# Kernel tuning notes

Hardware: AMD Instinct MI355X
Metric: run time of the kernel (lower is better)

## Reference

```python
import jax, jax.numpy as jnp
import numpy as np

N_HEAD = 12

def setup_inputs() -> dict:
    key = jax.random.key(0)
    k1, k2, k3 = jax.random.split(key, 3)
    B, T, E = 4, 2048, 768
    x = jax.random.normal(k1, (B, T, E), dtype=jnp.float32)
    Wqkv = jax.random.normal(k2, (E, 3 * E), dtype=jnp.float32) * 0.02
    Wproj = jax.random.normal(k3, (E, E), dtype=jnp.float32) * 0.02
    return {"x": x, "Wqkv": Wqkv, "Wproj": Wproj}

def reference(x, Wqkv, Wproj):
    B, T, E = x.shape
    H = N_HEAD
    hd = E // H
    qkv = x @ Wqkv                                  # [B,T,3E]
    q, k, v = jnp.split(qkv, 3, axis=-1)
    # [B,T,E] -> [B,H,T,hd]
    q = q.reshape(B, T, H, hd).transpose(0, 2, 1, 3)
    k = k.reshape(B, T, H, hd).transpose(0, 2, 1, 3)
    v = v.reshape(B, T, H, hd).transpose(0, 2, 1, 3)
    scores = jnp.einsum("bhqd,bhkd->bhqk", q, k) / jnp.sqrt(jnp.float32(hd))
    # original: masked_fill(tril(scores)==0, -inf) == causal mask (upper triangle zeroed by tril)
    masked = jnp.where(jnp.tril(scores) == 0, -jnp.inf, scores)
    attn = jax.nn.softmax(masked, axis=-1)
    out = jnp.einsum("bhqk,bhkd->bhqd", attn, v)    # [B,H,T,hd]
    out = out.transpose(0, 2, 1, 3).reshape(B, T, E)
    return out @ Wproj
```

## Files before the change

### kernel.cpp

```cpp
#include <hip/hip_runtime.h>
#include <hip/hip_bf16.h>


#define BB 4
#define TT 2048
#define EE 768
#define HH 12
#define HD 64
#define KK 768
#define BTE (BB*TT*EE)

typedef __attribute__((ext_vector_type(8))) short bf16x8;
typedef __attribute__((ext_vector_type(4))) float f32x4;
typedef __attribute__((ext_vector_type(16))) float f32x16;
typedef __attribute__((ext_vector_type(4))) int i32x4;

#define QSC 0.18033688011112042f

#define GLOAD16(gp, lp) \
    __builtin_amdgcn_global_load_lds( \
        (const __attribute__((address_space(1))) unsigned*)(gp), \
        (__attribute__((address_space(3))) unsigned*)(lp), 16, 0, 0)

static __device__ __forceinline__ unsigned short f2bf(float f) {
    unsigned u = __builtin_bit_cast(unsigned, f);
    u += 0x7fffu + ((u >> 16) & 1u);
    return (unsigned short)(u >> 16);
}

static __device__ __forceinline__ unsigned cvt_pk_bf16(float lo, float hi) {
    unsigned r;
    asm("v_cvt_pk_bf16_f32 %0, %1, %2" : "=v"(r) : "v"(lo), "v"(hi));
    return r;
}

__global__ __launch_bounds__(256)
void convx_kernel(const float* __restrict__ x, unsigned short* __restrict__ xb) {
    const size_t i = ((size_t)blockIdx.x * 256 + threadIdx.x) * 8;
    float4 a = *(const float4*)&x[i];
    float4 b = *(const float4*)&x[i + 4];
    ushort4 lo, hi;
    lo.x = f2bf(a.x); lo.y = f2bf(a.y); lo.z = f2bf(a.z); lo.w = f2bf(a.w);
    hi.x = f2bf(b.x); hi.y = f2bf(b.y); hi.z = f2bf(b.z); hi.w = f2bf(b.w);
    *(ushort4*)&xb[i] = lo;
    *(ushort4*)&xb[i + 4] = hi;
}

__global__ __launch_bounds__(256)
void transw_kernel(const float* __restrict__ W, unsigned short* __restrict__ Wt, int N) {
    __shared__ unsigned short Ts[64][72];
    const int n0 = blockIdx.x * 64;
    const int k0 = blockIdx.y * 64;
    const int tid = threadIdx.x;
    {
        const int r = tid >> 4;
        const int c4 = (tid & 15) << 2;
#pragma unroll
        for (int i = 0; i < 4; ++i) {
            const int k = r + i * 16;
            float4 w4 = *(const float4*)&W[(size_t)(k0 + k) * N + n0 + c4];
            Ts[k][c4 + 0] = f2bf(w4.x); Ts[k][c4 + 1] = f2bf(w4.y);
            Ts[k][c4 + 2] = f2bf(w4.z); Ts[k][c4 + 3] = f2bf(w4.w);
        }
    }
    __syncthreads();
#pragma unroll
    for (int i = 0; i < 2; ++i) {
        const int idx = tid + i * 256;
        const int n = idx >> 3;
        const int ch = idx & 7;
        ushort4 p0, p1;
        p0.x = Ts[ch * 8 + 0][n]; p0.y = Ts[ch * 8 + 1][n];
        p0.z = Ts[ch * 8 + 2][n]; p0.w = Ts[ch * 8 + 3][n];
        p1.x = Ts[ch * 8 + 4][n]; p1.y = Ts[ch * 8 + 5][n];
        p1.z = Ts[ch * 8 + 6][n]; p1.w = Ts[ch * 8 + 7][n];
        *(ushort4*)&Wt[(size_t)(n0 + n) * KK + k0 + ch * 8] = p0;
        *(ushort4*)&Wt[(size_t)(n0 + n) * KK + k0 + ch * 8 + 4] = p1;
    }
}

template<int MODE>
__global__ __launch_bounds__(256)
void mfma_gemm_kernel(const unsigned short* __restrict__ A,
                      const unsigned short* __restrict__ Wt,
                      unsigned short* __restrict__ q_ws,
                      unsigned short* __restrict__ k_ws,
                      unsigned short* __restrict__ v_ws,
                      float* __restrict__ outf) {
    __shared__ __align__(16) unsigned short As[3][8 * 512];
    __shared__ __align__(16) unsigned short Bs[3][8 * 512];

    const int nwg = gridDim.x * gridDim.y;
    const int orig = blockIdx.y * gridDim.x + blockIdx.x;
    const int cpx = nwg >> 3;
    const int swz = (orig & 7) * cpx + (orig >> 3);
    const int bx = swz % gridDim.x;
    const int by = swz / gridDim.x;

    const int tid = threadIdx.x;
    const int w = tid >> 6, lane = tid & 63;
    const int c = lane & 15, g = lane >> 4;
    const int wr = w >> 1, wc = w & 1;
    const int m0 = by * 128, n0 = bx * 128;

    const int lrow16 = lane & 15;
    const int lch16  = (lane >> 4) * 8;

    const unsigned short* Ap = A  + (size_t)m0 * KK;
    const unsigned short* Bp = Wt + (size_t)n0 * KK;

    f32x4 acc[4][4] = {};
    const int NT = KK / 32;

#define GSTAGE(pp, kt_) do { const int k0_ = (kt_) * 32; const int f0_ = 2 * w; \
        GLOAD16(Ap + (size_t)(f0_ * 16      + lrow16) * KK + k0_ + lch16, &As[pp][(f0_    ) * 512]); \
        GLOAD16(Ap + (size_t)((f0_ + 1) * 16 + lrow16) * KK + k0_ + lch16, &As[pp][(f0_ + 1) * 512]); \
        GLOAD16(Bp + (size_t)(f0_ * 16      + lrow16) * KK + k0_ + lch16, &Bs[pp][(f0_    ) * 512]); \
        GLOAD16(Bp + (size_t)((f0_ + 1) * 16 + lrow16) * KK + k0_ + lch16, &Bs[pp][(f0_ + 1) * 512]); \
    } while (0)

    GSTAGE(0, 0);
    GSTAGE(1, 1);

    for (int kt = 0; kt < NT; ++kt) {
        if (kt < NT - 1) asm volatile("s_waitcnt vmcnt(4)" ::: "memory");
        else             asm volatile("s_waitcnt vmcnt(0)" ::: "memory");
        __builtin_amdgcn_s_barrier();
        __builtin_amdgcn_sched_barrier(0);
        asm volatile("" ::: "memory");

        if (kt + 2 < NT) GSTAGE((kt + 2) % 3, kt + 2);

        const int p = kt % 3;
        bf16x8 af[4], bfr[4];
#pragma unroll
        for (int m = 0; m < 4; ++m)
            af[m] = *(const bf16x8*)&As[p][(wr * 4 + m) * 512 + lane * 8];
#pragma unroll
        for (int n = 0; n < 4; ++n)
            bfr[n] = *(const bf16x8*)&Bs[p][(wc * 4 + n) * 512 + lane * 8];
#pragma unroll
        for (int m = 0; m < 4; ++m)
#pragma unroll
            for (int n = 0; n < 4; ++n)
                acc[m][n] = __builtin_amdgcn_mfma_f32_16x16x32_bf16(af[m], bfr[n], acc[m][n], 0, 0, 0);
    }
#undef GSTAGE

    if (MODE == 0) {
        const int which = n0 / EE;
        const int hh = (n0 % EE) / HD + wc;
        const int bb = m0 / TT;
        const int tb = (m0 % TT) + wr * 64;
        const int bh = bb * HH + hh;
        if (which < 2) {
            const float sc_ = (which == 0) ? QSC : 1.0f;
            unsigned short* dst = (which == 0) ? q_ws : k_ws;
#pragma unroll
            for (int m = 0; m < 4; ++m) {
                const int t32 = (tb >> 5) + (m >> 1);
#pragma unroll
                for (int n = 0; n < 4; ++n) {
                    unsigned short* base = dst
                        + ((size_t)(bh * (TT / 32) + t32) * 4 + n) * 512
                        + ((m & 1) * 16 + 4 * g + 32 * (c >> 3)) * 8 + (c & 7);
#pragma unroll
                    for (int j = 0; j < 4; ++j)
                        base[j * 8] = f2bf(acc[m][n][j] * sc_);
                }
            }
        } else {
            unsigned short* vb = v_ws + ((size_t)(bh * (TT / 64) + (tb >> 6))) * 4096;
#pragma unroll
            for (int m = 0; m < 4; ++m)
#pragma unroll
                for (int n = 0; n < 4; ++n) {
                    unsigned short* base = vb + ((size_t)(n >> 1) * 4 + m) * 512
                        + ((n & 1) * 16 + c + 32 * (g >> 1)) * 8 + 4 * (g & 1);
                    ushort4 pk;
                    pk.x = f2bf(acc[m][n][0]); pk.y = f2bf(acc[m][n][1]);
                    pk.z = f2bf(acc[m][n][2]); pk.w = f2bf(acc[m][n][3]);
                    *(ushort4*)base = pk;
                }
        }
    } else {
#pragma unroll
        for (int m = 0; m < 4; ++m)
#pragma unroll
            for (int n = 0; n < 4; ++n)
#pragma unroll
                for (int j = 0; j < 4; ++j)
                    outf[(size_t)(m0 + wr * 64 + m * 16 + 4 * g + j) * EE
                         + n0 + wc * 64 + n * 16 + c] = acc[m][n][j];
    }
}

__global__ __launch_bounds__(64)
void attn_kernel(const unsigned short* __restrict__ qf,
                 const unsigned short* __restrict__ kfr,
                 const unsigned short* __restrict__ vfr,
                 unsigned short* __restrict__ attn_b) {
    const int bh = blockIdx.x;
    const int j = (TT / 32 - 1) - (int)blockIdx.y;
    const int b = bh / HH, h = bh % HH;
    const int lane = threadIdx.x;
    const int lq = lane & 31;
    const int hiL = lane >> 5;

    const int q0 = j * 32;
    const int qg = q0 + lq;

    const unsigned short* qbase = qf + ((size_t)(bh * (TT / 32) + j)) * 2048;
    bf16x8 qa[4];
#pragma unroll
    for (int ds = 0; ds < 4; ++ds)
        qa[ds] = *(const bf16x8*)&qbase[ds * 512 + lane * 8];

    const unsigned short* kfb = kfr + (size_t)bh * 131072;
    const unsigned short* vfb = vfr + (size_t)bh * 131072;

    const i32x4 onesw = {0x3F803F80, 0x3F803F80, 0x3F803F80, 0x3F803F80};
    const bf16x8 ones = __builtin_bit_cast(bf16x8, onesw);

    f32x16 o0 = {}, o1 = {}, ol = {};

    const int ktiles = (j >> 1) + 1;

    for (int kt = 0; kt < ktiles; ++kt) {
        const int kv0 = kt * 64;

        bf16x8 kf[8], vf[8];
        {
            const unsigned short* kc = kfb + ((size_t)(2 * kt) * 4) * 512 + lane * 8;
#pragma unroll
            for (int ch = 0; ch < 8; ++ch)
                kf[ch] = *(const bf16x8*)&kc[ch * 512];
            const unsigned short* vc = vfb + (size_t)kt * 4096 + lane * 8;
#pragma unroll
            for (int ch = 0; ch < 8; ++ch)
                vf[ch] = *(const bf16x8*)&vc[ch * 512];
        }

        f32x16 s0 = {}, s1 = {};
        __builtin_amdgcn_s_setprio(1);
#pragma unroll
        for (int ds = 0; ds < 4; ++ds) {
            s0 = __builtin_amdgcn_mfma_f32_32x32x16_bf16(kf[ds],     qa[ds], s0, 0, 0, 0);
            s1 = __builtin_amdgcn_mfma_f32_32x32x16_bf16(kf[4 + ds], qa[ds], s1, 0, 0, 0);
        }
        __builtin_amdgcn_s_setprio(0);

        if (kv0 + 63 > q0) {
#pragma unroll
            for (int r = 0; r < 16; ++r) {
                const int crow = (r & 3) + 8 * (r >> 2) + 4 * hiL;
                if (kv0 + crow > qg)      s0[r] = -INFINITY;
                if (kv0 + 32 + crow > qg) s1[r] = -INFINITY;
            }
        }

#pragma unroll
        for (int r = 0; r < 16; ++r) s0[r] = __builtin_amdgcn_exp2f(s0[r]);
#pragma unroll
        for (int r = 0; r < 16; ++r) s1[r] = __builtin_amdgcn_exp2f(s1[r]);

        __builtin_amdgcn_s_setprio(1);
#define PACKSTEP(E0,E1,E2,E3,E4,E5,E6,E7, VK) do { \
        unsigned a0 = cvt_pk_bf16(E0, E1); \
        unsigned a1 = cvt_pk_bf16(E2, E3); \
        unsigned b0 = cvt_pk_bf16(E4, E5); \
        unsigned b1 = cvt_pk_bf16(E6, E7); \
        asm("v_permlane32_swap_b32 %0, %1" : "+v"(a0), "+v"(b0)); \
        asm("v_permlane32_swap_b32 %0, %1" : "+v"(a1), "+v"(b1)); \
        i32x4 pw; \
        pw[0] = (int)a0; pw[1] = (int)a1; pw[2] = (int)b0; pw[3] = (int)b1; \
        const bf16x8 pa = __builtin_bit_cast(bf16x8, pw); \
        o0 = __builtin_amdgcn_mfma_f32_32x32x16_bf16(pa, vf[VK],     o0, 0, 0, 0); \
        o1 = __builtin_amdgcn_mfma_f32_32x32x16_bf16(pa, vf[4 + VK], o1, 0, 0, 0); \
        ol = __builtin_amdgcn_mfma_f32_32x32x16_bf16(pa, ones,       ol, 0, 0, 0); \
    } while (0)

        PACKSTEP(s0[0], s0[1], s0[2], s0[3], s0[4], s0[5], s0[6], s0[7], 0);
        PACKSTEP(s0[8], s0[9], s0[10], s0[11], s0[12], s0[13], s0[14], s0[15], 1);
        PACKSTEP(s1[0], s1[1], s1[2], s1[3], s1[4], s1[5], s1[6], s1[7], 2);
        PACKSTEP(s1[8], s1[9], s1[10], s1[11], s1[12], s1[13], s1[14], s1[15], 3);
#undef PACKSTEP
        __builtin_amdgcn_s_setprio(0);
    }

    unsigned short* op = attn_b + ((size_t)b * TT + q0) * EE + h * HD;
#pragma unroll
    for (int r = 0; r < 16; ++r) {
        const int crow = (r & 3) + 8 * (r >> 2) + 4 * hiL;
        const float li = 1.f / ol[r];
        op[(size_t)crow * EE + lq]      = f2bf(o0[r] * li);
        op[(size_t)crow * EE + 32 + lq] = f2bf(o1[r] * li);
    }
}

extern "C" void kernel_launch(void* const* d_in, const int* in_sizes, int n_in,
                              void* d_out, int out_size, void* d_ws, size_t ws_size,
                              hipStream_t stream) {
    const float* x     = (const float*)d_in[0];
    const float* wqkv  = (const float*)d_in[1];
    const float* wproj = (const float*)d_in[2];
    float* out = (float*)d_out;

    unsigned short* ws = (unsigned short*)d_ws;
    unsigned short* q_ws    = ws;
    unsigned short* k_ws    = ws + (size_t)BTE;
    unsigned short* v_ws    = ws + 2 * (size_t)BTE;
    unsigned short* xb      = ws + 3 * (size_t)BTE;
    unsigned short* attn_b  = ws + 4 * (size_t)BTE;
    unsigned short* wqkv_t  = ws + 5 * (size_t)BTE;
    unsigned short* wproj_t = wqkv_t + (size_t)2304 * 768;

    convx_kernel<<<BTE / 2048, 256, 0, stream>>>(x, xb);
    transw_kernel<<<dim3(2304 / 64, KK / 64), 256, 0, stream>>>(wqkv, wqkv_t, 2304);
    transw_kernel<<<dim3(768 / 64, KK / 64), 256, 0, stream>>>(wproj, wproj_t, 768);

    mfma_gemm_kernel<0><<<dim3(2304 / 128, 8192 / 128), 256, 0, stream>>>(
        xb, wqkv_t, q_ws, k_ws, v_ws, nullptr);
    attn_kernel<<<dim3(BB * HH, TT / 32), 64, 0, stream>>>(q_ws, k_ws, v_ws, attn_b);
    mfma_gemm_kernel<1><<<dim3(EE / 128, 8192 / 128), 256, 0, stream>>>(
        attn_b, wproj_t, nullptr, nullptr, nullptr, out);
}
```

Baseline: 149.6 us.

## Store GEMM operands in pre-tiled fragment layout for contiguous LDS loads

The x conversion, weight transpose and attention output now write bf16 operands in a 16x32 fragment-tiled layout, 512 contiguous elements per tile. The GEMM's global-to-LDS loads then read one fully contiguous 1 KB block per wave instead of 16 strided rows. This is meant to improve global load coalescing in both projection GEMMs. In exchange, the attention epilogue scatters bf16 stores in a more fragmented pattern.

```diff
diff --git a/kernel.cpp b/kernel.cpp
--- a/kernel.cpp
+++ b/kernel.cpp
@@ -35,19 +35,29 @@
 }
 
 __global__ __launch_bounds__(256)
-void convx_kernel(const float* __restrict__ x, unsigned short* __restrict__ xb) {
-    const size_t i = ((size_t)blockIdx.x * 256 + threadIdx.x) * 8;
-    float4 a = *(const float4*)&x[i];
-    float4 b = *(const float4*)&x[i + 4];
-    ushort4 lo, hi;
-    lo.x = f2bf(a.x); lo.y = f2bf(a.y); lo.z = f2bf(a.z); lo.w = f2bf(a.w);
-    hi.x = f2bf(b.x); hi.y = f2bf(b.y); hi.z = f2bf(b.z); hi.w = f2bf(b.w);
-    *(ushort4*)&xb[i] = lo;
-    *(ushort4*)&xb[i + 4] = hi;
+void convx_kernel(const float* __restrict__ x, unsigned short* __restrict__ xf) {
+    const int t16 = blockIdx.x;
+    const int tid = threadIdx.x;
+    const int l = tid & 63;
+    const int row = t16 * 16 + (l & 15);
+    const int kbase = (l >> 4) << 3;
+#pragma unroll
+    for (int pass = 0; pass < 6; ++pass) {
+        const int kb = (tid >> 6) + 4 * pass;
+        const int k = kb * 32 + kbase;
+        float4 a = *(const float4*)&x[(size_t)row * KK + k];
+        float4 b = *(const float4*)&x[(size_t)row * KK + k + 4];
+        ushort4 lo, hi;
+        lo.x = f2bf(a.x); lo.y = f2bf(a.y); lo.z = f2bf(a.z); lo.w = f2bf(a.w);
+        hi.x = f2bf(b.x); hi.y = f2bf(b.y); hi.z = f2bf(b.z); hi.w = f2bf(b.w);
+        unsigned short* dst = &xf[((size_t)t16 * 24 + kb) * 512 + l * 8];
+        *(ushort4*)dst = lo;
+        *(ushort4*)(dst + 4) = hi;
+    }
 }
 
 __global__ __launch_bounds__(256)
-void transw_kernel(const float* __restrict__ W, unsigned short* __restrict__ Wt, int N) {
+void transw_kernel(const float* __restrict__ W, unsigned short* __restrict__ Wf, int N) {
     __shared__ unsigned short Ts[64][72];
     const int n0 = blockIdx.x * 64;
     const int k0 = blockIdx.y * 64;
@@ -67,22 +77,28 @@
 #pragma unroll
     for (int i = 0; i < 2; ++i) {
         const int idx = tid + i * 256;
-        const int n = idx >> 3;
-        const int ch = idx & 7;
+        const int sub = idx >> 6;
+        const int l = idx & 63;
+        const int n16l = sub & 3, kbl = sub >> 2;
+        const int nloc = n16l * 16 + (l & 15);
+        const int kloc = kbl * 32 + ((l >> 4) << 3);
         ushort4 p0, p1;
-        p0.x = Ts[ch * 8 + 0][n]; p0.y = Ts[ch * 8 + 1][n];
-        p0.z = Ts[ch * 8 + 2][n]; p0.w = Ts[ch * 8 + 3][n];
-        p1.x = Ts[ch * 8 + 4][n]; p1.y = Ts[ch * 8 + 5][n];
-        p1.z = Ts[ch * 8 + 6][n]; p1.w = Ts[ch * 8 + 7][n];
-        *(ushort4*)&Wt[(size_t)(n0 + n) * KK + k0 + ch * 8] = p0;
-        *(ushort4*)&Wt[(size_t)(n0 + n) * KK + k0 + ch * 8 + 4] = p1;
+        p0.x = Ts[kloc + 0][nloc]; p0.y = Ts[kloc + 1][nloc];
+        p0.z = Ts[kloc + 2][nloc]; p0.w = Ts[kloc + 3][nloc];
+        p1.x = Ts[kloc + 4][nloc]; p1.y = Ts[kloc + 5][nloc];
+        p1.z = Ts[kloc + 6][nloc]; p1.w = Ts[kloc + 7][nloc];
+        const int n16 = (n0 >> 4) + n16l;
+        const int kb  = (k0 >> 5) + kbl;
+        unsigned short* dst = &Wf[((size_t)n16 * 24 + kb) * 512 + l * 8];
+        *(ushort4*)dst = p0;
+        *(ushort4*)(dst + 4) = p1;
     }
 }
 
 template<int MODE>
 __global__ __launch_bounds__(256)
-void mfma_gemm_kernel(const unsigned short* __restrict__ A,
-                      const unsigned short* __restrict__ Wt,
+void mfma_gemm_kernel(const unsigned short* __restrict__ Af,
+                      const unsigned short* __restrict__ Bf,
                       unsigned short* __restrict__ q_ws,
                       unsigned short* __restrict__ k_ws,
                       unsigned short* __restrict__ v_ws,
@@ -103,20 +119,17 @@
     const int wr = w >> 1, wc = w & 1;
     const int m0 = by * 128, n0 = bx * 128;
 
-    const int lrow16 = lane & 15;
-    const int lch16  = (lane >> 4) * 8;
-
-    const unsigned short* Ap = A  + (size_t)m0 * KK;
-    const unsigned short* Bp = Wt + (size_t)n0 * KK;
+    const unsigned short* Ap = Af + ((size_t)(m0 >> 4) * 24) * 512;
+    const unsigned short* Bp = Bf + ((size_t)(n0 >> 4) * 24) * 512;
 
     f32x4 acc[4][4] = {};
     const int NT = KK / 32;
 
-#define GSTAGE(pp, kt_) do { const int k0_ = (kt_) * 32; const int f0_ = 2 * w; \
-        GLOAD16(Ap + (size_t)(f0_ * 16      + lrow16) * KK + k0_ + lch16, &As[pp][(f0_    ) * 512]); \
-        GLOAD16(Ap + (size_t)((f0_ + 1) * 16 + lrow16) * KK + k0_ + lch16, &As[pp][(f0_ + 1) * 512]); \
-        GLOAD16(Bp + (size_t)(f0_ * 16      + lrow16) * KK + k0_ + lch16, &Bs[pp][(f0_    ) * 512]); \
-        GLOAD16(Bp + (size_t)((f0_ + 1) * 16 + lrow16) * KK + k0_ + lch16, &Bs[pp][(f0_ + 1) * 512]); \
+#define GSTAGE(pp, kt_) do { const int f0_ = 2 * w; \
+        GLOAD16(Ap + ((size_t)(f0_    ) * 24 + (kt_)) * 512 + lane * 8, &As[pp][(f0_    ) * 512]); \
+        GLOAD16(Ap + ((size_t)(f0_ + 1) * 24 + (kt_)) * 512 + lane * 8, &As[pp][(f0_ + 1) * 512]); \
+        GLOAD16(Bp + ((size_t)(f0_    ) * 24 + (kt_)) * 512 + lane * 8, &Bs[pp][(f0_    ) * 512]); \
+        GLOAD16(Bp + ((size_t)(f0_ + 1) * 24 + (kt_)) * 512 + lane * 8, &Bs[pp][(f0_ + 1) * 512]); \
     } while (0)
 
     GSTAGE(0, 0);
@@ -199,7 +212,7 @@
 void attn_kernel(const unsigned short* __restrict__ qf,
                  const unsigned short* __restrict__ kfr,
                  const unsigned short* __restrict__ vfr,
-                 unsigned short* __restrict__ attn_b) {
+                 unsigned short* __restrict__ attn_f) {
     const int bh = blockIdx.x;
     const int j = (TT / 32 - 1) - (int)blockIdx.y;
     const int b = bh / HH, h = bh % HH;
@@ -288,13 +301,16 @@
         __builtin_amdgcn_s_setprio(0);
     }
 
-    unsigned short* op = attn_b + ((size_t)b * TT + q0) * EE + h * HD;
+    const int rbase = b * TT + q0;
 #pragma unroll
     for (int r = 0; r < 16; ++r) {
         const int crow = (r & 3) + 8 * (r >> 2) + 4 * hiL;
         const float li = 1.f / ol[r];
-        op[(size_t)crow * EE + lq]      = f2bf(o0[r] * li);
-        op[(size_t)crow * EE + 32 + lq] = f2bf(o1[r] * li);
+        const int t16 = (rbase + crow) >> 4;
+        const int lA = (crow & 15) + 16 * (lq >> 3);
+        const int e  = lq & 7;
+        attn_f[((size_t)t16 * 24 + (h * 2 + 0)) * 512 + lA * 8 + e] = f2bf(o0[r] * li);
+        attn_f[((size_t)t16 * 24 + (h * 2 + 1)) * 512 + lA * 8 + e] = f2bf(o1[r] * li);
     }
 }
 
@@ -310,18 +326,18 @@
     unsigned short* q_ws    = ws;
     unsigned short* k_ws    = ws + (size_t)BTE;
     unsigned short* v_ws    = ws + 2 * (size_t)BTE;
-    unsigned short* xb      = ws + 3 * (size_t)BTE;
-    unsigned short* attn_b  = ws + 4 * (size_t)BTE;
-    unsigned short* wqkv_t  = ws + 5 * (size_t)BTE;
-    unsigned short* wproj_t = wqkv_t + (size_t)2304 * 768;
-
-    convx_kernel<<<BTE / 2048, 256, 0, stream>>>(x, xb);
-    transw_kernel<<<dim3(2304 / 64, KK / 64), 256, 0, stream>>>(wqkv, wqkv_t, 2304);
-    transw_kernel<<<dim3(768 / 64, KK / 64), 256, 0, stream>>>(wproj, wproj_t, 768);
+    unsigned short* xf      = ws + 3 * (size_t)BTE;
+    unsigned short* attn_f  = ws + 4 * (size_t)BTE;
+    unsigned short* wqkv_f  = ws + 5 * (size_t)BTE;
+    unsigned short* wproj_f = wqkv_f + (size_t)2304 * 768;
+
+    convx_kernel<<<TT * BB / 16, 256, 0, stream>>>(x, xf);
+    transw_kernel<<<dim3(2304 / 64, KK / 64), 256, 0, stream>>>(wqkv, wqkv_f, 2304);
+    transw_kernel<<<dim3(768 / 64, KK / 64), 256, 0, stream>>>(wproj, wproj_f, 768);
 
     mfma_gemm_kernel<0><<<dim3(2304 / 128, 8192 / 128), 256, 0, stream>>>(
-        xb, wqkv_t, q_ws, k_ws, v_ws, nullptr);
-    attn_kernel<<<dim3(BB * HH, TT / 32), 64, 0, stream>>>(q_ws, k_ws, v_ws, attn_b);
+        xf, wqkv_f, q_ws, k_ws, v_ws, nullptr);
+    attn_kernel<<<dim3(BB * HH, TT / 32), 64, 0, stream>>>(q_ws, k_ws, v_ws, attn_f);
     mfma_gemm_kernel<1><<<dim3(EE / 128, 8192 / 128), 256, 0, stream>>>(
-        attn_b, wproj_t, nullptr, nullptr, nullptr, out);
-}
+        attn_f, wproj_f, nullptr, nullptr, nullptr, out);
+}
```

New measurement: 124.1 us. 1.21x faster.
